# Kernel tuning notes

Measured on AMD Instinct MI355X. Metric: run time of the kernel, lower is better.

## Reference

```python
import jax, jax.numpy as jnp
import numpy as np

N, S, D = 16, 32, 256      # batch, seq_len, hidden_size
B = 4                      # sample_size (Monte-Carlo beams)
CH = 4 * D                 # cell_hidden_dim = 4*hidden (hard-coded in __init__)
EPS = 1e-20


def _ln(x, g, b):
    m = x.mean(-1, keepdims=True)
    v = ((x - m) ** 2).mean(-1, keepdims=True)
    return (x - m) / jnp.sqrt(v + 1e-5) * g + b


def _masked_softmax(logits, mask):
    p = jax.nn.softmax(logits, axis=-1)
    p = p * mask + EPS
    return p / p.sum(-1, keepdims=True)


def _cell(l, r, w1, b1, w2, b2, ln2_g, ln2_b):
    # TreeLSTM-style fused cell: Linear -> GELU -> Linear -> gates -> LayerNorm
    cat = jnp.concatenate([l, r], axis=-1)                  # (NB, s, 2D)
    inter = jax.nn.gelu(cat @ w1 + b1, approximate=False)   # (NB, s, 4D)
    contents = (inter @ w2 + b2).reshape(*l.shape[:-1], 4, D)
    gates = jax.nn.sigmoid(contents[..., 0:3, :])
    f1, f2, ig = gates[..., 0, :], gates[..., 1, :], gates[..., 2, :]
    parent = contents[..., 3, :]
    return _ln(f1 * l + f2 * r + ig * parent, ln2_g, ln2_b)


def _select(old_h, new_h, mask, accu, dec_W, dec_b, key):
    NB, Sc, Dd = new_h.shape
    old_l, old_r = old_h[:, :-1], old_h[:, 1:]
    nh = new_h * mask[:, :, None]
    pad = jnp.zeros((NB, 1, Dd), nh.dtype)
    l1 = jnp.concatenate([pad, nh[:, :-1]], axis=1)
    l2 = jnp.concatenate([pad, l1[:, :-1]], axis=1)
    r1 = jnp.concatenate([nh[:, 1:], pad], axis=1)
    r2 = jnp.concatenate([r1[:, 1:], pad], axis=1)
    win = jnp.concatenate([l2, l1, nh, r1, r2], axis=-1)    # (NB, Sc, 5D)
    logits = (win @ dec_W + dec_b)[..., 0] / np.sqrt(5 * Dd)
    # straight-through Gumbel softmax (temperature = 1)
    u = jax.random.uniform(key, logits.shape, logits.dtype)
    g = -jnp.log(-jnp.log(u + EPS) + EPS)
    y_soft = _masked_softmax(logits + g, mask)
    y_hard = jax.nn.one_hot(jnp.argmax(y_soft, axis=-1), Sc, dtype=y_soft.dtype)
    sel = jax.lax.stop_gradient(y_hard - y_soft) + y_soft
    soft_scores = jnp.sum(sel * _masked_softmax(logits, mask), axis=1)
    accu = accu + jnp.log(soft_scores + EPS)
    cs = jnp.cumsum(sel, axis=1)
    left = (1.0 - cs)[:, :, None]
    right = (cs - sel)[:, :, None]
    merged = sel[:, :, None] * new_h + left * old_l + right * old_r
    return merged, accu


def setup_inputs() -> dict:
    key = jax.random.key(0)
    ks = jax.random.split(key, 6)
    f32 = jnp.float32
    return {
        "x": jax.random.normal(ks[0], (N, S, D), f32),
        "input_mask": jnp.ones((N, S), f32),
        "word_W": jax.random.normal(ks[1], (D, D), f32) / np.sqrt(D),
        "word_b": jnp.zeros((D,), f32),
        "ln_g": jnp.ones((D,), f32),
        "ln_b": jnp.zeros((D,), f32),
        "w1": jax.random.normal(ks[2], (2 * D, CH), f32) / np.sqrt(2 * D),
        "b1": jnp.zeros((CH,), f32),
        "w2": jax.random.normal(ks[3], (CH, 4 * D), f32) / np.sqrt(CH),
        "b2": jnp.zeros((4 * D,), f32),
        "ln2_g": jnp.ones((D,), f32),
        "ln2_b": jnp.zeros((D,), f32),
        "dec_W": jax.random.normal(ks[4], (5 * D, 1), f32) / np.sqrt(5 * D),
        "dec_b": jnp.zeros((1,), f32),
    }


def reference(x, input_mask, word_W, word_b, ln_g, ln_b, w1, b1, w2, b2,
              ln2_g, ln2_b, dec_W, dec_b):
    state = _ln(x @ word_W + word_b, ln_g, ln_b)                 # (N, S, D)
    state = jnp.repeat(state[:, None], B, axis=1).reshape(N * B, S, D)
    lmask = jnp.repeat(input_mask[:, None], B, axis=1).reshape(N * B, S)
    accu = jnp.zeros((N * B,), state.dtype)
    base = jax.random.key(1234)
    # sequential tree-building recurrence; sequence axis shrinks by 1 each step
    for i in range(S - 1):
        l, r = state[:, :-1], state[:, 1:]
        new_state = _cell(l, r, w1, b1, w2, b2, ln2_g, ln2_b)
        if i < S - 2:
            new_state, new_accu = _select(state, new_state, lmask[:, i + 1:],
                                          accu, dec_W, dec_b,
                                          jax.random.fold_in(base, i))
        else:
            new_accu = accu
        done = lmask[:, i + 1]
        state = done[:, None, None] * new_state + (1.0 - done[:, None, None]) * state[:, :-1]
        accu = done * new_accu + (1.0 - done) * accu
    h = state[:, 0].reshape(N, B, D)
    scores = jax.nn.softmax(accu.reshape(N, B, 1), axis=1)
    return jnp.sum(scores * h, axis=1)                            # (N, D)
```

## Files before the change

kernel.cpp:

```cpp
#include <hip/hip_runtime.h>
#include <cstdint>
#include <cstddef>

namespace {
constexpr int kP0 = 31;
constexpr int kM0 = 496;
}

__device__ float g_state[2][64 * 32 * 256];
__device__ float g_nh[2][64 * kP0 * 256];
__device__ float g_s5[2][64 * kP0 * 5];
__device__ float g_nh0[kM0 * 256];
__device__ float g_s50[kM0 * 5];
__device__ float g_inter0[(size_t)kM0 * 1024];
__device__ float g_cont0[(size_t)kM0 * 1024];
__device__ float g_p1[4][128 * 1024];
__device__ float g_p2[4][128 * 1024];
__device__ float g_accu[64];
__device__ int g_slots[2][128];

__device__ __forceinline__ void tf2x32(uint32_t k0, uint32_t k1, uint32_t x0,
                                       uint32_t x1, uint32_t& o0, uint32_t& o1) {
  uint32_t ks2 = k0 ^ k1 ^ 0x1BD11BDAu;
  x0 += k0; x1 += k1;
#define TF_ROT(v, r) (((v) << (r)) | ((v) >> (32 - (r))))
#define TF_RD(r) { x0 += x1; x1 = TF_ROT(x1, r); x1 ^= x0; }
  TF_RD(13) TF_RD(15) TF_RD(26) TF_RD(6)   x0 += k1;  x1 += ks2 + 1u;
  TF_RD(17) TF_RD(29) TF_RD(16) TF_RD(24)  x0 += ks2; x1 += k0 + 2u;
  TF_RD(13) TF_RD(15) TF_RD(26) TF_RD(6)   x0 += k0;  x1 += k1 + 3u;
  TF_RD(17) TF_RD(29) TF_RD(16) TF_RD(24)  x0 += k1;  x1 += ks2 + 4u;
  TF_RD(13) TF_RD(15) TF_RD(26) TF_RD(6)   x0 += ks2; x1 += k0 + 5u;
  o0 = x0; o1 = x1;
#undef TF_RD
#undef TF_ROT
}

__device__ __forceinline__ float blockSum256(float v, float* red4, int tid) {
#pragma unroll
  for (int o = 32; o > 0; o >>= 1) v += __shfl_down(v, o, 64);
  __syncthreads();
  if ((tid & 63) == 0) red4[tid >> 6] = v;
  __syncthreads();
  return red4[0] + red4[1] + red4[2] + red4[3];
}
__device__ __forceinline__ float waveMax64(float v) {
#pragma unroll
  for (int o = 32; o > 0; o >>= 1) v = fmaxf(v, __shfl_xor(v, o, 64));
  return v;
}
__device__ __forceinline__ float waveSum64(float v) {
#pragma unroll
  for (int o = 32; o > 0; o >>= 1) v += __shfl_xor(v, o, 64);
  return v;
}
__device__ __forceinline__ float geluf(float v) {
  return 0.5f * v * (1.0f + erff(v * 0.70710678118654752440f));
}

__global__ __launch_bounds__(256) void k_embed(const float* __restrict__ x,
                                               const float* __restrict__ wW,
                                               const float* __restrict__ wb,
                                               const float* __restrict__ lng,
                                               const float* __restrict__ lnb) {
  int row = blockIdx.x;
  int d = threadIdx.x;
  __shared__ float xs[256];
  __shared__ float red4[4];
  xs[d] = x[row * 256 + d];
  __syncthreads();
  float acc = wb[d];
  for (int k = 0; k < 256; ++k) acc = fmaf(xs[k], wW[k * 256 + d], acc);
  float mean = blockSum256(acc, red4, d) * (1.0f / 256.0f);
  float cen = acc - mean;
  float var = blockSum256(cen * cen, red4, d) * (1.0f / 256.0f);
  float o = cen / sqrtf(var + 1e-5f) * lng[d] + lnb[d];
  int n = row >> 5, s = row & 31;
#pragma unroll
  for (int bb = 0; bb < 4; ++bb)
    g_state[0][((n * 4 + bb) * 32 + s) * 256 + d] = o;
  if (row == 0 && d < 64) g_accu[d] = 0.0f;
}


__global__ __launch_bounds__(256) void k_g1s(const float* __restrict__ w1,
                                             const float* __restrict__ b1) {
  __shared__ float As[64][33];
  __shared__ float Ws[64][68];
  const int tid = threadIdx.x;
  const int colB = blockIdx.x * 64;
  const int rowB = blockIdx.y * 32;
  const int row = tid & 15, cg = tid >> 4;
  const int ar = tid >> 4, ak = (tid & 15) * 4;
  const float *Ab0, *Ab1;
  {
    int m0 = rowB + ar; if (m0 > kM0 - 1) m0 = kM0 - 1;
    int m1 = rowB + ar + 16; if (m1 > kM0 - 1) m1 = kM0 - 1;
    int n0 = m0 / 31, j0 = m0 - n0 * 31;
    int n1 = m1 / 31, j1 = m1 - n1 * 31;
    Ab0 = g_state[0] + (n0 * 4) * 8192 + j0 * 256;
    Ab1 = g_state[0] + (n1 * 4) * 8192 + j1 * 256;
  }
  float4 aR0 = *(const float4*)&Ab0[ak];
  float4 aR1 = *(const float4*)&Ab1[ak];
  float4 wR[4];
#pragma unroll
  for (int q = 0; q < 4; ++q) {
    int f = tid + q * 256; int kk = f >> 4, c4 = f & 15;
    wR[q] = *(const float4*)&w1[(size_t)kk * 1024 + colB + c4 * 4];
  }
  float acc0[4] = {}, acc1[4] = {};
  for (int c = 0; c < 8; ++c) {
    As[ak + 0][ar] = aR0.x; As[ak + 1][ar] = aR0.y; As[ak + 2][ar] = aR0.z; As[ak + 3][ar] = aR0.w;
    As[ak + 0][ar + 16] = aR1.x; As[ak + 1][ar + 16] = aR1.y; As[ak + 2][ar + 16] = aR1.z; As[ak + 3][ar + 16] = aR1.w;
#pragma unroll
    for (int q = 0; q < 4; ++q) {
      int f = tid + q * 256; int kk = f >> 4, c4 = f & 15;
      *(float4*)&Ws[kk][c4 * 4] = wR[q];
    }
    __syncthreads();
    if (c < 7) {
      int kb = (c + 1) * 64;
      aR0 = *(const float4*)&Ab0[kb + ak];
      aR1 = *(const float4*)&Ab1[kb + ak];
#pragma unroll
      for (int q = 0; q < 4; ++q) {
        int f = tid + q * 256; int kk = f >> 4, c4 = f & 15;
        wR[q] = *(const float4*)&w1[(size_t)(kb + kk) * 1024 + colB + c4 * 4];
      }
    }
#pragma unroll
    for (int kk = 0; kk < 64; ++kk) {
      float a0 = As[kk][row], a1 = As[kk][row + 16];
      float4 w = *(const float4*)&Ws[kk][cg * 4];
      acc0[0] = fmaf(a0, w.x, acc0[0]); acc0[1] = fmaf(a0, w.y, acc0[1]);
      acc0[2] = fmaf(a0, w.z, acc0[2]); acc0[3] = fmaf(a0, w.w, acc0[3]);
      acc1[0] = fmaf(a1, w.x, acc1[0]); acc1[1] = fmaf(a1, w.y, acc1[1]);
      acc1[2] = fmaf(a1, w.z, acc1[2]); acc1[3] = fmaf(a1, w.w, acc1[3]);
    }
    __syncthreads();
  }
  int col = colB + cg * 4;
  float4 bb = *(const float4*)&b1[col];
  int m0 = rowB + row, m1 = rowB + row + 16;
  if (m0 < kM0) {
    float4 o;
    o.x = geluf(acc0[0] + bb.x); o.y = geluf(acc0[1] + bb.y);
    o.z = geluf(acc0[2] + bb.z); o.w = geluf(acc0[3] + bb.w);
    *(float4*)&g_inter0[(size_t)m0 * 1024 + col] = o;
  }
  if (m1 < kM0) {
    float4 o;
    o.x = geluf(acc1[0] + bb.x); o.y = geluf(acc1[1] + bb.y);
    o.z = geluf(acc1[2] + bb.z); o.w = geluf(acc1[3] + bb.w);
    *(float4*)&g_inter0[(size_t)m1 * 1024 + col] = o;
  }
}

__global__ __launch_bounds__(256) void k_g2s(const float* __restrict__ w2) {
  __shared__ float As[64][33];
  __shared__ float Ws[64][68];
  const int tid = threadIdx.x;
  const int colB = blockIdx.x * 64;
  const int rowB = blockIdx.y * 32;
  const int row = tid & 15, cg = tid >> 4;
  const int ar = tid >> 4, ak = (tid & 15) * 4;
  int m0s = rowB + ar; if (m0s > kM0 - 1) m0s = kM0 - 1;
  int m1s = rowB + ar + 16; if (m1s > kM0 - 1) m1s = kM0 - 1;
  const float* Ab0 = g_inter0 + (size_t)m0s * 1024;
  const float* Ab1 = g_inter0 + (size_t)m1s * 1024;
  float4 aR0 = *(const float4*)&Ab0[ak];
  float4 aR1 = *(const float4*)&Ab1[ak];
  float4 wR[4];
#pragma unroll
  for (int q = 0; q < 4; ++q) {
    int f = tid + q * 256; int kk = f >> 4, c4 = f & 15;
    wR[q] = *(const float4*)&w2[(size_t)kk * 1024 + colB + c4 * 4];
  }
  float acc0[4] = {}, acc1[4] = {};
  for (int c = 0; c < 16; ++c) {
    As[ak + 0][ar] = aR0.x; As[ak + 1][ar] = aR0.y; As[ak + 2][ar] = aR0.z; As[ak + 3][ar] = aR0.w;
    As[ak + 0][ar + 16] = aR1.x; As[ak + 1][ar + 16] = aR1.y; As[ak + 2][ar + 16] = aR1.z; As[ak + 3][ar + 16] = aR1.w;
#pragma unroll
    for (int q = 0; q < 4; ++q) {
      int f = tid + q * 256; int kk = f >> 4, c4 = f & 15;
      *(float4*)&Ws[kk][c4 * 4] = wR[q];
    }
    __syncthreads();
    if (c < 15) {
      int kb = (c + 1) * 64;
      aR0 = *(const float4*)&Ab0[kb + ak];
      aR1 = *(const float4*)&Ab1[kb + ak];
#pragma unroll
      for (int q = 0; q < 4; ++q) {
        int f = tid + q * 256; int kk = f >> 4, c4 = f & 15;
        wR[q] = *(const float4*)&w2[(size_t)(kb + kk) * 1024 + colB + c4 * 4];
      }
    }
#pragma unroll
    for (int kk = 0; kk < 64; ++kk) {
      float a0 = As[kk][row], a1 = As[kk][row + 16];
      float4 w = *(const float4*)&Ws[kk][cg * 4];
      acc0[0] = fmaf(a0, w.x, acc0[0]); acc0[1] = fmaf(a0, w.y, acc0[1]);
      acc0[2] = fmaf(a0, w.z, acc0[2]); acc0[3] = fmaf(a0, w.w, acc0[3]);
      acc1[0] = fmaf(a1, w.x, acc1[0]); acc1[1] = fmaf(a1, w.y, acc1[1]);
      acc1[2] = fmaf(a1, w.z, acc1[2]); acc1[3] = fmaf(a1, w.w, acc1[3]);
    }
    __syncthreads();
  }
  int col = colB + cg * 4;
  int m0 = rowB + row, m1 = rowB + row + 16;
  if (m0 < kM0) {
    float4 o = {acc0[0], acc0[1], acc0[2], acc0[3]};
    *(float4*)&g_cont0[(size_t)m0 * 1024 + col] = o;
  }
  if (m1 < kM0) {
    float4 o = {acc1[0], acc1[1], acc1[2], acc1[3]};
    *(float4*)&g_cont0[(size_t)m1 * 1024 + col] = o;
  }
}

__global__ __launch_bounds__(256) void k_g1t(const float* __restrict__ w1, int buf) {
  __shared__ float As[64][33];
  __shared__ float Ws[64][68];
  const int tid = threadIdx.x;
  const int colB = blockIdx.x * 64;
  const int rowB = blockIdx.y * 32;
  const int Ks = blockIdx.z;
  const int kb0 = Ks * 128;
  const int row = tid & 15, cg = tid >> 4;
  const int ar = tid >> 4, ak = (tid & 15) * 4;
  const float *Ab0, *Ab1;
  {
    int s0 = rowB + ar, s1 = rowB + ar + 16;
    int j0 = g_slots[buf][s0]; if (j0 < 0) j0 = 0;
    int j1 = g_slots[buf][s1]; if (j1 < 0) j1 = 0;
    Ab0 = g_state[buf] + (s0 >> 1) * 8192 + j0 * 256;
    Ab1 = g_state[buf] + (s1 >> 1) * 8192 + j1 * 256;
  }
  float4 aR0 = *(const float4*)&Ab0[kb0 + ak];
  float4 aR1 = *(const float4*)&Ab1[kb0 + ak];
  float4 wR[4];
#pragma unroll
  for (int q = 0; q < 4; ++q) {
    int f = tid + q * 256; int kk = f >> 4, c4 = f & 15;
    wR[q] = *(const float4*)&w1[(size_t)(kb0 + kk) * 1024 + colB + c4 * 4];
  }
  float acc0[4] = {}, acc1[4] = {};
  for (int c = 0; c < 2; ++c) {
    As[ak + 0][ar] = aR0.x; As[ak + 1][ar] = aR0.y; As[ak + 2][ar] = aR0.z; As[ak + 3][ar] = aR0.w;
    As[ak + 0][ar + 16] = aR1.x; As[ak + 1][ar + 16] = aR1.y; As[ak + 2][ar + 16] = aR1.z; As[ak + 3][ar + 16] = aR1.w;
#pragma unroll
    for (int q = 0; q < 4; ++q) {
      int f = tid + q * 256; int kk = f >> 4, c4 = f & 15;
      *(float4*)&Ws[kk][c4 * 4] = wR[q];
    }
    __syncthreads();
    if (c < 1) {
      int kb = kb0 + 64;
      aR0 = *(const float4*)&Ab0[kb + ak];
      aR1 = *(const float4*)&Ab1[kb + ak];
#pragma unroll
      for (int q = 0; q < 4; ++q) {
        int f = tid + q * 256; int kk = f >> 4, c4 = f & 15;
        wR[q] = *(const float4*)&w1[(size_t)(kb + kk) * 1024 + colB + c4 * 4];
      }
    }
#pragma unroll
    for (int kk = 0; kk < 64; ++kk) {
      float a0 = As[kk][row], a1 = As[kk][row + 16];
      float4 w = *(const float4*)&Ws[kk][cg * 4];
      acc0[0] = fmaf(a0, w.x, acc0[0]); acc0[1] = fmaf(a0, w.y, acc0[1]);
      acc0[2] = fmaf(a0, w.z, acc0[2]); acc0[3] = fmaf(a0, w.w, acc0[3]);
      acc1[0] = fmaf(a1, w.x, acc1[0]); acc1[1] = fmaf(a1, w.y, acc1[1]);
      acc1[2] = fmaf(a1, w.z, acc1[2]); acc1[3] = fmaf(a1, w.w, acc1[3]);
    }
    __syncthreads();
  }
  int col = colB + cg * 4;
  {
    float4 o = {acc0[0], acc0[1], acc0[2], acc0[3]};
    *(float4*)&g_p1[Ks][(rowB + row) * 1024 + col] = o;
  }
  {
    float4 o = {acc1[0], acc1[1], acc1[2], acc1[3]};
    *(float4*)&g_p1[Ks][(rowB + row + 16) * 1024 + col] = o;
  }
}

__device__ __forceinline__ float4 g2t_loadA(int grow, int kpos, const float* __restrict__ b1) {
  size_t g = (size_t)grow * 1024 + kpos;
  float4 p0 = *(const float4*)&g_p1[0][g];
  float4 p1 = *(const float4*)&g_p1[1][g];
  float4 p2 = *(const float4*)&g_p1[2][g];
  float4 p3 = *(const float4*)&g_p1[3][g];
  float4 bb = *(const float4*)&b1[kpos];
  float4 r;
  r.x = geluf(p0.x + p1.x + p2.x + p3.x + bb.x);
  r.y = geluf(p0.y + p1.y + p2.y + p3.y + bb.y);
  r.z = geluf(p0.z + p1.z + p2.z + p3.z + bb.z);
  r.w = geluf(p0.w + p1.w + p2.w + p3.w + bb.w);
  return r;
}

__global__ __launch_bounds__(256) void k_g2t(const float* __restrict__ w2,
                                             const float* __restrict__ b1) {
  __shared__ float As[64][33];
  __shared__ float Ws[64][68];
  const int tid = threadIdx.x;
  const int colB = blockIdx.x * 64;
  const int rowB = blockIdx.y * 32;
  const int Ks = blockIdx.z;
  const int kb0 = Ks * 256;
  const int row = tid & 15, cg = tid >> 4;
  const int ar = tid >> 4, ak = (tid & 15) * 4;
  const int grow0 = rowB + ar, grow1 = rowB + ar + 16;
  float4 aR0 = g2t_loadA(grow0, kb0 + ak, b1);
  float4 aR1 = g2t_loadA(grow1, kb0 + ak, b1);
  float4 wR[4];
#pragma unroll
  for (int q = 0; q < 4; ++q) {
    int f = tid + q * 256; int kk = f >> 4, c4 = f & 15;
    wR[q] = *(const float4*)&w2[(size_t)(kb0 + kk) * 1024 + colB + c4 * 4];
  }
  float acc0[4] = {}, acc1[4] = {};
  for (int c = 0; c < 4; ++c) {
    As[ak + 0][ar] = aR0.x; As[ak + 1][ar] = aR0.y; As[ak + 2][ar] = aR0.z; As[ak + 3][ar] = aR0.w;
    As[ak + 0][ar + 16] = aR1.x; As[ak + 1][ar + 16] = aR1.y; As[ak + 2][ar + 16] = aR1.z; As[ak + 3][ar + 16] = aR1.w;
#pragma unroll
    for (int q = 0; q < 4; ++q) {
      int f = tid + q * 256; int kk = f >> 4, c4 = f & 15;
      *(float4*)&Ws[kk][c4 * 4] = wR[q];
    }
    __syncthreads();
    if (c < 3) {
      int kb = kb0 + (c + 1) * 64;
      aR0 = g2t_loadA(grow0, kb + ak, b1);
      aR1 = g2t_loadA(grow1, kb + ak, b1);
#pragma unroll
      for (int q = 0; q < 4; ++q) {
        int f = tid + q * 256; int kk = f >> 4, c4 = f & 15;
        wR[q] = *(const float4*)&w2[(size_t)(kb + kk) * 1024 + colB + c4 * 4];
      }
    }
#pragma unroll
    for (int kk = 0; kk < 64; ++kk) {
      float a0 = As[kk][row], a1 = As[kk][row + 16];
      float4 w = *(const float4*)&Ws[kk][cg * 4];
      acc0[0] = fmaf(a0, w.x, acc0[0]); acc0[1] = fmaf(a0, w.y, acc0[1]);
      acc0[2] = fmaf(a0, w.z, acc0[2]); acc0[3] = fmaf(a0, w.w, acc0[3]);
      acc1[0] = fmaf(a1, w.x, acc1[0]); acc1[1] = fmaf(a1, w.y, acc1[1]);
      acc1[2] = fmaf(a1, w.z, acc1[2]); acc1[3] = fmaf(a1, w.w, acc1[3]);
    }
    __syncthreads();
  }
  int col = colB + cg * 4;
  {
    float4 o = {acc0[0], acc0[1], acc0[2], acc0[3]};
    *(float4*)&g_p2[Ks][(rowB + row) * 1024 + col] = o;
  }
  {
    float4 o = {acc1[0], acc1[1], acc1[2], acc1[3]};
    *(float4*)&g_p2[Ks][(rowB + row + 16) * 1024 + col] = o;
  }
}

__global__ __launch_bounds__(256) void k_cellfull(const float* __restrict__ imask,
                                                  const float* __restrict__ ln2g,
                                                  const float* __restrict__ ln2b,
                                                  const float* __restrict__ decW,
                                                  const float* __restrict__ b2) {
  int m = blockIdx.x;
  int d = threadIdx.x;
  int n = m / 31, j = m - n * 31;
  const float* st = g_state[0] + (n * 4) * 8192;
  const float* crow = g_cont0 + (size_t)m * 1024;
  float c0 = crow[d] + b2[d];
  float c1 = crow[256 + d] + b2[256 + d];
  float c2 = crow[512 + d] + b2[512 + d];
  float c3 = crow[768 + d] + b2[768 + d];
  float l = st[j * 256 + d];
  float r = st[(j + 1) * 256 + d];
  float f1 = 1.0f / (1.0f + expf(-c0));
  float f2 = 1.0f / (1.0f + expf(-c1));
  float ig = 1.0f / (1.0f + expf(-c2));
  float pre = f1 * l + f2 * r + ig * c3;
  __shared__ float red4[4];
  __shared__ float w5[4][5];
  float mean = blockSum256(pre, red4, d) * (1.0f / 256.0f);
  float cen = pre - mean;
  float var = blockSum256(cen * cen, red4, d) * (1.0f / 256.0f);
  float nh = cen / sqrtf(var + 1e-5f) * ln2g[d] + ln2b[d];
  g_nh0[m * 256 + d] = nh;
  float mv = imask[n * 32 + 1 + j];
  float nhm = nh * mv;
  float pv[5];
#pragma unroll
  for (int t = 0; t < 5; ++t) pv[t] = nhm * decW[t * 256 + d];
#pragma unroll
  for (int t = 0; t < 5; ++t)
#pragma unroll
    for (int o = 32; o > 0; o >>= 1) pv[t] += __shfl_down(pv[t], o, 64);
  __syncthreads();
  if ((d & 63) == 0) {
#pragma unroll
    for (int t = 0; t < 5; ++t) w5[d >> 6][t] = pv[t];
  }
  __syncthreads();
  if (d < 5) g_s50[m * 5 + d] = w5[0][d] + w5[1][d] + w5[2][d] + w5[3][d];
}

__global__ __launch_bounds__(256) void k_cellmerge(
    const float* __restrict__ imask, const float* __restrict__ decW,
    const float* __restrict__ decb, const float* __restrict__ b2,
    const float* __restrict__ ln2g, const float* __restrict__ ln2b,
    int i, int last) {
  const int b = blockIdx.x, grp = blockIdx.y;
  const int tid = threadIdx.x, st = tid, lane = tid & 63, wv = tid >> 6;
  const int Sc = 31 - i;
  const int buf = i & 1;
  const int n32 = (b >> 2) * 32;
  __shared__ float sh_nhf[2][256];
  __shared__ float sh_s5f[2][5];
  __shared__ float red4[4];
  __shared__ float w5s[4][5];
  __shared__ int sh_k;
  __shared__ float sh_sv;
  int slot0 = -1, slot1 = -1;
  if (i > 0) { slot0 = g_slots[buf][2 * b]; slot1 = g_slots[buf][2 * b + 1]; }
  const float* s5Src = (i == 0) ? (g_s50 + (b >> 2) * kP0 * 5) : (g_s5[buf] + b * kP0 * 5);
  const float* nhSrcG = (i == 0) ? (g_nh0 + (size_t)(b >> 2) * kP0 * 256)
                                 : (g_nh[buf] + (size_t)b * kP0 * 256);
  const float* stOld = g_state[buf] + b * 8192;
  float* stNew = g_state[(i + 1) & 1] + b * 8192;
  float* nhDst = g_nh[(i + 1) & 1] + (size_t)b * kP0 * 256;
  float* s5Dst = g_s5[(i + 1) & 1] + b * kP0 * 5;
  float done = imask[n32 + i + 1];

  if (i > 0) {
#pragma unroll 1
    for (int s = 0; s < 2; ++s) {
      int j = (s == 0) ? slot0 : slot1;
      if (j < 0) continue;
      int sr = 2 * b + s;
      float c[4];
#pragma unroll
      for (int q = 0; q < 4; ++q) {
        int g = sr * 1024 + q * 256 + st;
        float v = ((g_p2[0][g] + g_p2[1][g]) + g_p2[2][g]) + g_p2[3][g];
        c[q] = v + b2[q * 256 + st];
      }
      float l = stOld[j * 256 + st];
      float r = stOld[(j + 1) * 256 + st];
      float f1 = 1.0f / (1.0f + expf(-c[0]));
      float f2 = 1.0f / (1.0f + expf(-c[1]));
      float ig = 1.0f / (1.0f + expf(-c[2]));
      float pre = f1 * l + f2 * r + ig * c[3];
      float mean = blockSum256(pre, red4, st) * (1.0f / 256.0f);
      float cen = pre - mean;
      float var = blockSum256(cen * cen, red4, st) * (1.0f / 256.0f);
      float nh = cen / sqrtf(var + 1e-5f) * ln2g[st] + ln2b[st];
      sh_nhf[s][st] = nh;
      float mv = imask[n32 + i + 1 + j];
      float nhm = nh * mv;
      float pv[5];
#pragma unroll
      for (int t = 0; t < 5; ++t) pv[t] = nhm * decW[t * 256 + st];
#pragma unroll
      for (int t = 0; t < 5; ++t) {
        float v = pv[t];
#pragma unroll
        for (int o = 32; o > 0; o >>= 1) v += __shfl_down(v, o, 64);
        pv[t] = v;
      }
      __syncthreads();
      if (lane == 0) {
#pragma unroll
        for (int t = 0; t < 5; ++t) w5s[wv][t] = pv[t];
      }
      __syncthreads();
      if (st < 5) sh_s5f[s][st] = w5s[0][st] + w5s[1][st] + w5s[2][st] + w5s[3][st];
    }
  }
  __syncthreads();

  if (!last && tid < 64) {
    int j = lane;
    bool act = j < Sc;
    float mv = 0.f, lg = 0.f;
    if (act) {
      mv = imask[n32 + i + 1 + j];
      float t5 = decb[0];
      if (j >= 2) {
        int rw = j - 2;
        t5 += (i > 0 && rw == slot0) ? sh_s5f[0][0] : (i > 0 && rw == slot1) ? sh_s5f[1][0] : s5Src[rw * 5 + 0];
      }
      if (j >= 1) {
        int rw = j - 1;
        t5 += (i > 0 && rw == slot0) ? sh_s5f[0][1] : (i > 0 && rw == slot1) ? sh_s5f[1][1] : s5Src[rw * 5 + 1];
      }
      {
        int rw = j;
        t5 += (i > 0 && rw == slot0) ? sh_s5f[0][2] : (i > 0 && rw == slot1) ? sh_s5f[1][2] : s5Src[rw * 5 + 2];
      }
      if (j + 1 < Sc) {
        int rw = j + 1;
        t5 += (i > 0 && rw == slot0) ? sh_s5f[0][3] : (i > 0 && rw == slot1) ? sh_s5f[1][3] : s5Src[rw * 5 + 3];
      }
      if (j + 2 < Sc) {
        int rw = j + 2;
        t5 += (i > 0 && rw == slot0) ? sh_s5f[0][4] : (i > 0 && rw == slot1) ? sh_s5f[1][4] : s5Src[rw * 5 + 4];
      }
      lg = t5 / 35.77708763999664f;
    }
    uint32_t fk0, fk1, o0, o1;
    tf2x32(0u, 1234u, 0u, (uint32_t)i, fk0, fk1);
    uint32_t idx = (uint32_t)(b * Sc + j);
    tf2x32(fk0, fk1, 0u, idx, o0, o1);
    uint32_t bits = o0 ^ o1;
    float u = __uint_as_float((bits >> 9) | 0x3f800000u) - 1.0f;
    float gum = -logf(-logf(u + 1e-20f) + 1e-20f);
    float z = lg + gum;
    float zm = waveMax64(act ? z : -3.0e38f);
    float e = act ? expf(z - zm) : 0.f;
    float p = e / waveSum64(e);
    float y = act ? (p * mv + 1e-20f) : 0.f;
    float ys = y / waveSum64(y);
    float av = act ? ys : -1.f;
    int ai = j;
#pragma unroll
    for (int o = 32; o > 0; o >>= 1) {
      float ov = __shfl_xor(av, o, 64);
      int oi = __shfl_xor(ai, o, 64);
      if (ov > av || (ov == av && oi < ai)) { av = ov; ai = oi; }
    }
    float lm = waveMax64(act ? lg : -3.0e38f);
    float e2 = act ? expf(lg - lm) : 0.f;
    float p2 = e2 / waveSum64(e2);
    float y2 = act ? (p2 * mv + 1e-20f) : 0.f;
    float ps = y2 / waveSum64(y2);
    float ysk = __shfl(ys, ai, 64);
    float psk = __shfl(ps, ai, 64);
    float sv = (1.0f - ysk) + ysk;
    if (j == 0) {
      sh_k = ai;
      sh_sv = sv;
      if (grp == 0) {
        g_accu[b] += done * logf(sv * psk + 1e-20f);
        int s0 = -1, s1 = -1;
        if (done != 0.0f) {
          if (ai >= 1) s0 = ai - 1;
          if (ai <= Sc - 2) s1 = ai;
        }
        g_slots[(i + 1) & 1][2 * b] = s0;
        g_slots[(i + 1) & 1][2 * b + 1] = s1;
      }
    }
  }
  __syncthreads();

  if (last) {
    if (grp == 0 && wv == 0) {
      float4 ol = *(const float4*)&stOld[lane * 4];
      float4 nh4;
      if (slot0 == 0) nh4 = *(const float4*)&sh_nhf[0][lane * 4];
      else if (slot1 == 0) nh4 = *(const float4*)&sh_nhf[1][lane * 4];
      else nh4 = *(const float4*)&nhSrcG[lane * 4];
      float4 o4;
      o4.x = done * nh4.x + (1.0f - done) * ol.x;
      o4.y = done * nh4.y + (1.0f - done) * ol.y;
      o4.z = done * nh4.z + (1.0f - done) * ol.z;
      o4.w = done * nh4.w + (1.0f - done) * ol.w;
      *(float4*)&stNew[lane * 4] = o4;
    }
    return;
  }

  int k = sh_k;
  float sv = sh_sv;
#pragma unroll 1
  for (int rr = 0; rr < 2; ++rr) {
    int jrow = grp * 8 + wv * 2 + rr;
    if (jrow >= Sc) continue;
    float4 ol = *(const float4*)&stOld[jrow * 256 + lane * 4];
    float4 ov4;
    if (done != 0.0f) {
      float4 mg;
      if (jrow < k) {
        mg = ol;
      } else if (jrow == k) {
        float4 nh4 = (i > 0 && k == slot0) ? *(const float4*)&sh_nhf[0][lane * 4]
                   : (i > 0 && k == slot1) ? *(const float4*)&sh_nhf[1][lane * 4]
                   : *(const float4*)&nhSrcG[k * 256 + lane * 4];
        mg.x = sv * nh4.x + (1.0f - sv) * ol.x;
        mg.y = sv * nh4.y + (1.0f - sv) * ol.y;
        mg.z = sv * nh4.z + (1.0f - sv) * ol.z;
        mg.w = sv * nh4.w + (1.0f - sv) * ol.w;
      } else {
        float4 orr = *(const float4*)&stOld[(jrow + 1) * 256 + lane * 4];
        mg.x = (1.0f - sv) * ol.x + sv * orr.x;
        mg.y = (1.0f - sv) * ol.y + sv * orr.y;
        mg.z = (1.0f - sv) * ol.z + sv * orr.z;
        mg.w = (1.0f - sv) * ol.w + sv * orr.w;
      }
      ov4.x = done * mg.x + (1.0f - done) * ol.x;
      ov4.y = done * mg.y + (1.0f - done) * ol.y;
      ov4.z = done * mg.z + (1.0f - done) * ol.z;
      ov4.w = done * mg.w + (1.0f - done) * ol.w;
    } else {
      ov4 = ol;
    }
    *(float4*)&stNew[jrow * 256 + lane * 4] = ov4;
    if (jrow < Sc - 1) {
      int src = (done != 0.0f && jrow > k) ? jrow + 1 : jrow;
      float4 nv = (i > 0 && src == slot0) ? *(const float4*)&sh_nhf[0][lane * 4]
                : (i > 0 && src == slot1) ? *(const float4*)&sh_nhf[1][lane * 4]
                : *(const float4*)&nhSrcG[src * 256 + lane * 4];
      *(float4*)&nhDst[jrow * 256 + lane * 4] = nv;
      float mv2 = imask[n32 + i + 2 + jrow];
      float pv[5];
#pragma unroll
      for (int t = 0; t < 5; ++t) {
        const float* dw = decW + t * 256 + lane * 4;
        pv[t] = (nv.x * dw[0] + nv.y * dw[1] + nv.z * dw[2] + nv.w * dw[3]) * mv2;
      }
#pragma unroll
      for (int t = 0; t < 5; ++t) {
        float v = pv[t];
#pragma unroll
        for (int o = 32; o > 0; o >>= 1) v += __shfl_down(v, o, 64);
        pv[t] = v;
      }
      if (lane == 0) {
#pragma unroll
        for (int t = 0; t < 5; ++t) s5Dst[jrow * 5 + t] = pv[t];
      }
    }
  }
}

__global__ __launch_bounds__(256) void k_final(float* __restrict__ out) {
  int n = blockIdx.x, d = threadIdx.x;
  float a0 = g_accu[n * 4 + 0], a1 = g_accu[n * 4 + 1];
  float a2 = g_accu[n * 4 + 2], a3 = g_accu[n * 4 + 3];
  float mx = fmaxf(fmaxf(a0, a1), fmaxf(a2, a3));
  float e0 = expf(a0 - mx), e1 = expf(a1 - mx), e2 = expf(a2 - mx), e3 = expf(a3 - mx);
  float ssum = e0 + e1 + e2 + e3;
  const float* st1 = g_state[1];
  float h0 = st1[(n * 4 + 0) * 8192 + d];
  float h1 = st1[(n * 4 + 1) * 8192 + d];
  float h2 = st1[(n * 4 + 2) * 8192 + d];
  float h3 = st1[(n * 4 + 3) * 8192 + d];
  out[n * 256 + d] = (e0 / ssum) * h0 + (e1 / ssum) * h1 + (e2 / ssum) * h2 + (e3 / ssum) * h3;
}

extern "C" void kernel_launch(void* const* d_in, const int* in_sizes, int n_in,
                              void* d_out, int out_size, void* d_ws, size_t ws_size,
                              hipStream_t stream) {
  (void)in_sizes; (void)n_in; (void)d_ws; (void)ws_size; (void)out_size;
  const float* x = (const float*)d_in[0];
  const float* imask = (const float*)d_in[1];
  const float* wW = (const float*)d_in[2];
  const float* wb = (const float*)d_in[3];
  const float* lng = (const float*)d_in[4];
  const float* lnb = (const float*)d_in[5];
  const float* w1 = (const float*)d_in[6];
  const float* b1 = (const float*)d_in[7];
  const float* w2 = (const float*)d_in[8];
  const float* b2 = (const float*)d_in[9];
  const float* ln2g = (const float*)d_in[10];
  const float* ln2b = (const float*)d_in[11];
  const float* decW = (const float*)d_in[12];
  const float* decb = (const float*)d_in[13];
  float* out = (float*)d_out;

  k_embed<<<dim3(512), dim3(256), 0, stream>>>(x, wW, wb, lng, lnb);
  k_g1s<<<dim3(16, 16), dim3(256), 0, stream>>>(w1, b1);
  k_g2s<<<dim3(16, 16), dim3(256), 0, stream>>>(w2);
  k_cellfull<<<dim3(kM0), dim3(256), 0, stream>>>(imask, ln2g, ln2b, decW, b2);
  k_cellmerge<<<dim3(64, 4), dim3(256), 0, stream>>>(imask, decW, decb, b2, ln2g, ln2b, 0, 0);
  for (int i = 1; i <= 30; ++i) {
    k_g1t<<<dim3(16, 4, 4), dim3(256), 0, stream>>>(w1, i & 1);
    k_g2t<<<dim3(16, 4, 4), dim3(256), 0, stream>>>(w2, b1);
    int lastf = (i == 30) ? 1 : 0;
    k_cellmerge<<<dim3(64, lastf ? 1 : 4), dim3(256), 0, stream>>>(imask, decW, decb, b2,
                                                                   ln2g, ln2b, i, lastf);
  }
  k_final<<<dim3(16), dim3(256), 0, stream>>>(out);
}
```

Baseline: 1.314 ms.

## Fuse first cell GEMM into merge kernel and swizzle setup GEMM tile order

```diff
diff --git a/kernel.cpp b/kernel.cpp
--- a/kernel.cpp
+++ b/kernel.cpp
@@ -87,8 +87,10 @@
   __shared__ float As[64][33];
   __shared__ float Ws[64][68];
   const int tid = threadIdx.x;
-  const int colB = blockIdx.x * 64;
-  const int rowB = blockIdx.y * 32;
+  const int wgid = blockIdx.x;
+  const int tsw = wgid >> 3;
+  const int colB = ((wgid & 7) + 8 * (tsw & 1)) * 64;
+  const int rowB = (tsw >> 1) * 32;
   const int row = tid & 15, cg = tid >> 4;
   const int ar = tid >> 4, ak = (tid & 15) * 4;
   const float *Ab0, *Ab1;
@@ -160,8 +162,10 @@
   __shared__ float As[64][33];
   __shared__ float Ws[64][68];
   const int tid = threadIdx.x;
-  const int colB = blockIdx.x * 64;
-  const int rowB = blockIdx.y * 32;
+  const int wgid = blockIdx.x;
+  const int tsw = wgid >> 3;
+  const int colB = ((wgid & 7) + 8 * (tsw & 1)) * 64;
+  const int rowB = (tsw >> 1) * 32;
   const int row = tid & 15, cg = tid >> 4;
   const int ar = tid >> 4, ak = (tid & 15) * 4;
   int m0s = rowB + ar; if (m0s > kM0 - 1) m0s = kM0 - 1;
@@ -216,74 +220,6 @@
   if (m1 < kM0) {
     float4 o = {acc1[0], acc1[1], acc1[2], acc1[3]};
     *(float4*)&g_cont0[(size_t)m1 * 1024 + col] = o;
-  }
-}
-
-__global__ __launch_bounds__(256) void k_g1t(const float* __restrict__ w1, int buf) {
-  __shared__ float As[64][33];
-  __shared__ float Ws[64][68];
-  const int tid = threadIdx.x;
-  const int colB = blockIdx.x * 64;
-  const int rowB = blockIdx.y * 32;
-  const int Ks = blockIdx.z;
-  const int kb0 = Ks * 128;
-  const int row = tid & 15, cg = tid >> 4;
-  const int ar = tid >> 4, ak = (tid & 15) * 4;
-  const float *Ab0, *Ab1;
-  {
-    int s0 = rowB + ar, s1 = rowB + ar + 16;
-    int j0 = g_slots[buf][s0]; if (j0 < 0) j0 = 0;
-    int j1 = g_slots[buf][s1]; if (j1 < 0) j1 = 0;
-    Ab0 = g_state[buf] + (s0 >> 1) * 8192 + j0 * 256;
-    Ab1 = g_state[buf] + (s1 >> 1) * 8192 + j1 * 256;
-  }
-  float4 aR0 = *(const float4*)&Ab0[kb0 + ak];
-  float4 aR1 = *(const float4*)&Ab1[kb0 + ak];
-  float4 wR[4];
-#pragma unroll
-  for (int q = 0; q < 4; ++q) {
-    int f = tid + q * 256; int kk = f >> 4, c4 = f & 15;
-    wR[q] = *(const float4*)&w1[(size_t)(kb0 + kk) * 1024 + colB + c4 * 4];
-  }
-  float acc0[4] = {}, acc1[4] = {};
-  for (int c = 0; c < 2; ++c) {
-    As[ak + 0][ar] = aR0.x; As[ak + 1][ar] = aR0.y; As[ak + 2][ar] = aR0.z; As[ak + 3][ar] = aR0.w;
-    As[ak + 0][ar + 16] = aR1.x; As[ak + 1][ar + 16] = aR1.y; As[ak + 2][ar + 16] = aR1.z; As[ak + 3][ar + 16] = aR1.w;
-#pragma unroll
-    for (int q = 0; q < 4; ++q) {
-      int f = tid + q * 256; int kk = f >> 4, c4 = f & 15;
-      *(float4*)&Ws[kk][c4 * 4] = wR[q];
-    }
-    __syncthreads();
-    if (c < 1) {
-      int kb = kb0 + 64;
-      aR0 = *(const float4*)&Ab0[kb + ak];
-      aR1 = *(const float4*)&Ab1[kb + ak];
-#pragma unroll
-      for (int q = 0; q < 4; ++q) {
-        int f = tid + q * 256; int kk = f >> 4, c4 = f & 15;
-        wR[q] = *(const float4*)&w1[(size_t)(kb + kk) * 1024 + colB + c4 * 4];
-      }
-    }
-#pragma unroll
-    for (int kk = 0; kk < 64; ++kk) {
-      float a0 = As[kk][row], a1 = As[kk][row + 16];
-      float4 w = *(const float4*)&Ws[kk][cg * 4];
-      acc0[0] = fmaf(a0, w.x, acc0[0]); acc0[1] = fmaf(a0, w.y, acc0[1]);
-      acc0[2] = fmaf(a0, w.z, acc0[2]); acc0[3] = fmaf(a0, w.w, acc0[3]);
-      acc1[0] = fmaf(a1, w.x, acc1[0]); acc1[1] = fmaf(a1, w.y, acc1[1]);
-      acc1[2] = fmaf(a1, w.z, acc1[2]); acc1[3] = fmaf(a1, w.w, acc1[3]);
-    }
-    __syncthreads();
-  }
-  int col = colB + cg * 4;
-  {
-    float4 o = {acc0[0], acc0[1], acc0[2], acc0[3]};
-    *(float4*)&g_p1[Ks][(rowB + row) * 1024 + col] = o;
-  }
-  {
-    float4 o = {acc1[0], acc1[1], acc1[2], acc1[3]};
-    *(float4*)&g_p1[Ks][(rowB + row + 16) * 1024 + col] = o;
   }
 }
 
@@ -409,11 +345,11 @@
   if (d < 5) g_s50[m * 5 + d] = w5[0][d] + w5[1][d] + w5[2][d] + w5[3][d];
 }
 
-__global__ __launch_bounds__(256) void k_cellmerge(
+__global__ __launch_bounds__(256) void k_cm(
     const float* __restrict__ imask, const float* __restrict__ decW,
     const float* __restrict__ decb, const float* __restrict__ b2,
     const float* __restrict__ ln2g, const float* __restrict__ ln2b,
-    int i, int last) {
+    const float* __restrict__ w1, int i, int last) {
   const int b = blockIdx.x, grp = blockIdx.y;
   const int tid = threadIdx.x, st = tid, lane = tid & 63, wv = tid >> 6;
   const int Sc = 31 - i;
@@ -421,6 +357,7 @@
   const int n32 = (b >> 2) * 32;
   __shared__ float sh_nhf[2][256];
   __shared__ float sh_s5f[2][5];
+  __shared__ float sA[3][256];
   __shared__ float red4[4];
   __shared__ float w5s[4][5];
   __shared__ int sh_k;
@@ -636,6 +573,54 @@
       }
     }
   }
+
+  if (done != 0.0f) {
+    __syncthreads();
+    {
+      int d = st;
+      float nhKv = (i > 0 && k == slot0) ? sh_nhf[0][d]
+                 : (i > 0 && k == slot1) ? sh_nhf[1][d]
+                 : nhSrcG[k * 256 + d];
+#pragma unroll
+      for (int t = 0; t < 3; ++t) {
+        int r = k - 1 + t;
+        if (r < 0 || r > Sc - 1) continue;
+        float ol = stOld[r * 256 + d];
+        float mg;
+        if (r < k) mg = ol;
+        else if (r == k) mg = sv * nhKv + (1.0f - sv) * ol;
+        else mg = (1.0f - sv) * ol + sv * stOld[(r + 1) * 256 + d];
+        sA[t][d] = done * mg + (1.0f - done) * ol;
+      }
+    }
+    __syncthreads();
+    const int has0 = (k >= 1);
+    const int has1 = (k <= Sc - 2);
+    const int kb0 = grp * 128;
+    const float* A0 = (grp < 2) ? sA[0] : sA[1];
+    const float* A1 = (grp < 2) ? sA[1] : sA[2];
+    const int koff = (grp < 2) ? kb0 : (kb0 - 256);
+    const int col = st * 4;
+    float a00 = 0.f, a01 = 0.f, a02 = 0.f, a03 = 0.f;
+    float a10 = 0.f, a11 = 0.f, a12 = 0.f, a13 = 0.f;
+    for (int kk = 0; kk < 128; ++kk) {
+      float4 w = *(const float4*)&w1[(size_t)(kb0 + kk) * 1024 + col];
+      float av0 = A0[koff + kk];
+      float av1 = A1[koff + kk];
+      a00 = fmaf(av0, w.x, a00); a01 = fmaf(av0, w.y, a01);
+      a02 = fmaf(av0, w.z, a02); a03 = fmaf(av0, w.w, a03);
+      a10 = fmaf(av1, w.x, a10); a11 = fmaf(av1, w.y, a11);
+      a12 = fmaf(av1, w.z, a12); a13 = fmaf(av1, w.w, a13);
+    }
+    if (has0) {
+      float4 o = {a00, a01, a02, a03};
+      *(float4*)&g_p1[grp][(2 * b + 0) * 1024 + col] = o;
+    }
+    if (has1) {
+      float4 o = {a10, a11, a12, a13};
+      *(float4*)&g_p1[grp][(2 * b + 1) * 1024 + col] = o;
+    }
+  }
 }
 
 __global__ __launch_bounds__(256) void k_final(float* __restrict__ out) {
@@ -674,16 +659,15 @@
   float* out = (float*)d_out;
 
   k_embed<<<dim3(512), dim3(256), 0, stream>>>(x, wW, wb, lng, lnb);
-  k_g1s<<<dim3(16, 16), dim3(256), 0, stream>>>(w1, b1);
-  k_g2s<<<dim3(16, 16), dim3(256), 0, stream>>>(w2);
+  k_g1s<<<dim3(256), dim3(256), 0, stream>>>(w1, b1);
+  k_g2s<<<dim3(256), dim3(256), 0, stream>>>(w2);
   k_cellfull<<<dim3(kM0), dim3(256), 0, stream>>>(imask, ln2g, ln2b, decW, b2);
-  k_cellmerge<<<dim3(64, 4), dim3(256), 0, stream>>>(imask, decW, decb, b2, ln2g, ln2b, 0, 0);
+  k_cm<<<dim3(64, 4), dim3(256), 0, stream>>>(imask, decW, decb, b2, ln2g, ln2b, w1, 0, 0);
   for (int i = 1; i <= 30; ++i) {
-    k_g1t<<<dim3(16, 4, 4), dim3(256), 0, stream>>>(w1, i & 1);
     k_g2t<<<dim3(16, 4, 4), dim3(256), 0, stream>>>(w2, b1);
     int lastf = (i == 30) ? 1 : 0;
-    k_cellmerge<<<dim3(64, lastf ? 1 : 4), dim3(256), 0, stream>>>(imask, decW, decb, b2,
-                                                                   ln2g, ln2b, i, lastf);
+    k_cm<<<dim3(64, lastf ? 1 : 4), dim3(256), 0, stream>>>(imask, decW, decb, b2,
+                                                            ln2g, ln2b, w1, i, lastf);
   }
   k_final<<<dim3(16), dim3(256), 0, stream>>>(out);
 }
```

Result: faster. 1.244 ms (-5.3%).
